# Kernel optimization log

Measured on AMD Instinct MI355X. Metric: run time of the kernel, lower is better.

## Reference

```python
import jax, jax.numpy as jnp
import numpy as np

# Static configuration matching the selected code path:
#   mode='inject_subject', is_self_attn=True, layer_id='up_blocks.0' (inject layer, bank hit)
#   alpha = AlphaScheduler.alpha(step=20, total=50, 'up_blocks.0') = 0.8 * 0.6 = 0.48
B, L, D, H = 4, 1024, 1280, 20
DH = D // H  # 64
ALPHA = 0.48


def setup_inputs() -> dict:
    key = jax.random.key(0)
    ks = jax.random.split(key, 8)
    w = lambda k, shp: (jax.random.normal(k, shp, dtype=jnp.float32) * 0.02)
    return {
        "hidden_states": jax.random.normal(ks[0], (B, L, D), dtype=jnp.float32),
        "Wq": w(ks[1], (D, D)),
        "Wk": w(ks[2], (D, D)),
        "Wv": w(ks[3], (D, D)),
        "Wo": w(ks[4], (D, D)),
        "bo": jnp.zeros((D,), dtype=jnp.float32),
        # cached background K/V, stored after head_to_batch_dim -> [B*H, L_bg, DH]
        "K_bg": jax.random.normal(ks[5], (B * H, L, DH), dtype=jnp.float32),
        "V_bg": jax.random.normal(ks[6], (B * H, L, DH), dtype=jnp.float32),
    }


def _head_to_batch(x):  # [B, L, D] -> [B*H, L, DH]
    b, l, _ = x.shape
    return x.reshape(b, l, H, DH).transpose(0, 2, 1, 3).reshape(b * H, l, DH)


def _batch_to_head(x):  # [B*H, L, DH] -> [B, L, D]
    bh, l, _ = x.shape
    b = bh // H
    return x.reshape(b, H, l, DH).transpose(0, 2, 1, 3).reshape(b, l, D)


def reference(hidden_states, Wq, Wk, Wv, Wo, bo, K_bg, V_bg):
    # q/k/v projections (self-attention: k, v from hidden_states)
    q = _head_to_batch(hidden_states @ Wq)  # [B*H, L, DH]
    k = _head_to_batch(hidden_states @ Wk)
    v = _head_to_batch(hidden_states @ Wv)

    # inject_subject: concat cached background K/V scaled by alpha along kv-seq dim
    k = jnp.concatenate([k, ALPHA * K_bg], axis=1)  # [B*H, 2L, DH]
    v = jnp.concatenate([v, ALPHA * V_bg], axis=1)

    # _sdpa: q scaled by scale*sqrt(dh), SDPA divides by sqrt(dh) -> net factor `scale`
    scale = 1.0 / jnp.sqrt(jnp.asarray(DH, dtype=q.dtype))
    scores = jnp.einsum('bqd,bkd->bqk', q, k) * scale  # [B*H, L, 2L]
    probs = jax.nn.softmax(scores, axis=-1)
    context = jnp.einsum('bqk,bkd->bqd', probs, v)  # [B*H, L, DH]

    out = _batch_to_head(context) @ Wo + bo  # to_out[0] linear
    return out
```

## Files before the change

kernel.cpp:

```cpp
#include <hip/hip_runtime.h>
#include <hip/hip_bf16.h>

#define B_   4
#define L_   1024
#define D_   1280
#define H_   20
#define DH_  64
#define BH_  (B_*H_)
#define L2_  (2*L_)
#define ALPHA_ 0.48f
#define QSCALE_ 0.180336880f

typedef __attribute__((ext_vector_type(8))) short short8;
typedef __attribute__((ext_vector_type(4))) float float4v;

__device__ __forceinline__ float exp2_fast(float x) {
    float r;
    asm volatile("v_exp_f32 %0, %1" : "=v"(r) : "v"(x));
    return r;
}

__device__ __forceinline__ ushort f2bf(float f) {
    union { float f; unsigned int i; } v; v.f = f;
    unsigned int i = v.i;
    unsigned int r = i + 0x7FFF + ((i >> 16) & 1);
    return (ushort)(r >> 16);
}
__device__ __forceinline__ short8 pack8(float4 f0, float4 f1) {
    short8 o;
    o[0] = (short)f2bf(f0.x); o[1] = (short)f2bf(f0.y);
    o[2] = (short)f2bf(f0.z); o[3] = (short)f2bf(f0.w);
    o[4] = (short)f2bf(f1.x); o[5] = (short)f2bf(f1.y);
    o[6] = (short)f2bf(f1.z); o[7] = (short)f2bf(f1.w);
    return o;
}
__device__ __forceinline__ void pack4_store(ushort* dst, float a, float b, float c, float d) {
    union { __hip_bfloat162 h; unsigned int u; } x, y;
    x.h = __float22bfloat162_rn(make_float2(a, b));
    y.h = __float22bfloat162_rn(make_float2(c, d));
    uint2 v; v.x = x.u; v.y = y.u;
    *(uint2*)dst = v;
}

__device__ __forceinline__ void async16(const void* g, void* l) {
    __builtin_amdgcn_global_load_lds(
        (__attribute__((address_space(1))) void*)g,
        (__attribute__((address_space(3))) void*)l, 16, 0, 0);
}

__global__ __launch_bounds__(256) void prep(
    const float* __restrict__ w0, const float* __restrict__ w1,
    const float* __restrict__ w2, const float* __restrict__ w3,
    ushort* __restrict__ Wt,
    const float* __restrict__ Vbg, ushort* __restrict__ Vt,
    const float* __restrict__ X, ushort* __restrict__ Xb,
    const float* __restrict__ Kbg, ushort* __restrict__ Kcv) {
    int bi = blockIdx.x, tid = threadIdx.x;
    __shared__ __align__(16) ushort t[64 * 72];
    if (bi < 2880) {
        bool doScale = (bi >= 1600);
        const float* src; int srcld; long sbase;
        ushort* dst = nullptr; int dstld = 0; long dbase = 0;
        ushort* vout = nullptr;
        if (bi < 1600) {
            int z = bi / 400, t4 = bi % 400;
            int by = t4 / 20, bx = t4 % 20;
            const float* srcs[4] = {w0, w1, w2, w3};
            src = srcs[z]; srcld = D_; dstld = D_;
            sbase = (long)(by * 64) * D_ + bx * 64;
            dst = Wt + (long)z * D_ * D_;
            dbase = (long)(bx * 64) * D_ + by * 64;
        } else {
            int j = bi - 1600;
            int bh = j >> 4, kt = j & 15;
            src = Vbg; srcld = DH_;
            sbase = ((long)bh * L_ + kt * 64) * DH_;
            vout = Vt + (((long)bh * 32 + 16 + kt) << 12);
        }
        int ldr = tid >> 3, ldc = (tid & 7) * 8;
#pragma unroll
        for (int i = 0; i < 2; i++) {
            int y = ldr + 32 * i;
            long idx = sbase + (long)y * srcld + ldc;
            float4 f0 = *(const float4*)&src[idx];
            float4 f1 = *(const float4*)&src[idx + 4];
            if (doScale) {
                f0.x *= ALPHA_; f0.y *= ALPHA_; f0.z *= ALPHA_; f0.w *= ALPHA_;
                f1.x *= ALPHA_; f1.y *= ALPHA_; f1.z *= ALPHA_; f1.w *= ALPHA_;
            }
            *(short8*)&t[y * 72 + ldc] = pack8(f0, f1);
        }
        __syncthreads();
        if (bi < 1600) {
            int r8 = (tid & 7) * 8, c0 = tid >> 3;
#pragma unroll
            for (int i = 0; i < 2; i++) {
                int c = c0 + i * 32;
                short8 o;
#pragma unroll
                for (int j2 = 0; j2 < 8; j2++) o[j2] = (short)t[(r8 + j2) * 72 + c];
                *(short8*)&dst[dbase + (long)c * dstld + r8] = o;
            }
        } else {
#pragma unroll
            for (int i = 0; i < 2; i++) {
                int jj = i * 256 + tid;
                int cc = jj >> 6, d2 = jj & 63;
                int rb = (cc >> 2) * 32 + (cc & 3) * 4;
                short8 o;
#pragma unroll
                for (int e = 0; e < 8; e++)
                    o[e] = (short)t[(rb + (e >> 2) * 16 + (e & 3)) * 72 + d2];
                *(short8*)&vout[(long)jj * 8] = o;
            }
        }
    } else if (bi < 5440) {
        long i = ((long)(bi - 2880) * 256 + tid) * 8;
        *(short8*)&Xb[i] = pack8(*(const float4*)&X[i], *(const float4*)&X[i + 4]);
    } else {
        int j2 = bi - 5440;
        int bh = j2 >> 4, kt = j2 & 15;
        const float* src = Kbg + ((long)bh * L_ + kt * 64) * DH_;
#pragma unroll
        for (int i = 0; i < 2; i++) {
            int r = i * 256 + tid;
            int kv = r >> 3, cd = r & 7;
            long idx = (long)kv * 64 + cd * 8;
            *(short8*)&t[kv * 72 + cd * 8] =
                pack8(*(const float4*)&src[idx], *(const float4*)&src[idx + 4]);
        }
        __syncthreads();
        ushort* outp = Kcv + (((long)bh * 16 + kt) << 12);
#pragma unroll
        for (int i = 0; i < 2; i++) {
            int jj = i * 256 + tid;
            int c = jj >> 6, kv = jj & 63;
            *(short8*)&outp[(long)jj * 8] = *(const short8*)&t[kv * 72 + c * 8];
        }
    }
}

template<int BMt, int BNt, int WROWS, int WCOLS>
__global__ __launch_bounds__(256) void gemm_tpl(
    const ushort* __restrict__ A, const ushort* __restrict__ Bt,
    ushort* __restrict__ Qp, ushort* __restrict__ Kp, ushort* __restrict__ Vt,
    float* __restrict__ Out, const float* __restrict__ bo, int mode) {
    constexpr int MI = BMt / WROWS / 16;
    constexpr int NI = BNt / WCOLS / 16;
    constexpr int ASZ = BMt * 32, BSZ = BNt * 32;
    constexpr int RB = 1280 / BNt;
    __shared__ __align__(16) ushort Al[2 * ASZ];
    __shared__ __align__(16) ushort Bl[2 * BSZ];
    int tid = threadIdx.x;
    int bx = blockIdx.x, by = blockIdx.y;
    int w = tid >> 6, lane = tid & 63, l15 = lane & 15, quad = lane >> 4;
    int wm = (w / WCOLS) * (BMt / WROWS);
    int wn = (w % WCOLS) * (BNt / WCOLS);
    float4v acc[MI][NI] = {};
    const int K = 1280;
    constexpr int NK = 40;
    const ushort* Arow = A + (long)by * BMt * K + (tid >> 2) * K + (tid & 3) * 8;
    const ushort* Brow = Bt + (long)bx * BNt * K + (tid >> 2) * K + (tid & 3) * 8;

    auto stage = [&](int ki, int b) {
#pragma unroll
        for (int i = 0; i < BMt / 64; i++)
            async16(Arow + (long)i * 64 * K + ki * 32, &Al[b * ASZ + (i * 4 + w) * 512]);
#pragma unroll
        for (int i = 0; i < BNt / 64; i++)
            async16(Brow + (long)i * 64 * K + ki * 32, &Bl[b * BSZ + (i * 4 + w) * 512]);
    };

    stage(0, 0);
    __syncthreads();
    for (int ki = 0; ki < NK; ki++) {
        int cur = ki & 1;
        if (ki + 1 < NK) stage(ki + 1, 1 - cur);
        short8 av[MI], bv[NI];
#pragma unroll
        for (int mi = 0; mi < MI; mi++)
            av[mi] = *(const short8*)&Al[cur * ASZ + (wm + mi * 16 + l15) * 32 + quad * 8];
#pragma unroll
        for (int ni = 0; ni < NI; ni++)
            bv[ni] = *(const short8*)&Bl[cur * BSZ + (wn + ni * 16 + l15) * 32 + quad * 8];
#pragma unroll
        for (int mi = 0; mi < MI; mi++)
#pragma unroll
            for (int ni = 0; ni < NI; ni++)
                acc[mi][ni] = __builtin_amdgcn_mfma_f32_16x16x32_bf16(av[mi], bv[ni], acc[mi][ni], 0, 0, 0);
        __syncthreads();
    }

    if (mode == 0) {
        int which = bx / RB;
#pragma unroll
        for (int mi = 0; mi < MI; mi++) {
            int m0 = by * BMt + wm + mi * 16 + quad * 4;
            int b = m0 >> 10, l0 = m0 & 1023;
#pragma unroll
            for (int ni = 0; ni < NI; ni++) {
                int n = bx * BNt + wn + ni * 16 + l15;
                int np = n - which * 1280;
                int h = np >> 6, dh = np & 63;
                if (which == 0) {
#pragma unroll
                    for (int r = 0; r < 4; r++)
                        Qp[((long)(b * H_ + h) * L_ + l0 + r) * DH_ + dh] =
                            f2bf(acc[mi][ni][r] * QSCALE_);
                } else if (which == 1) {
                    long kb = ((((long)(b * H_ + h) * 16 + (l0 >> 6)) * 8 + (dh >> 3)) * 64
                               + (l0 & 63)) * 8 + (dh & 7);
#pragma unroll
                    for (int r = 0; r < 4; r++)
                        Kp[kb + r * 8] = f2bf(acc[mi][ni][r]);
                } else {
                    int j = l0 & 63;
                    int cc = ((j >> 5) << 2) | ((j >> 2) & 3);
                    int eb = ((j >> 4) & 1) << 2;
                    pack4_store(&Vt[((((long)(b * H_ + h) * 32 + (l0 >> 6)) * 8
                                      + cc) * 64 + dh) * 8 + eb],
                                acc[mi][ni][0], acc[mi][ni][1],
                                acc[mi][ni][2], acc[mi][ni][3]);
                }
            }
        }
    } else {
#pragma unroll
        for (int mi = 0; mi < MI; mi++) {
            int mloc = wm + mi * 16 + quad * 4;
#pragma unroll
            for (int ni = 0; ni < NI; ni++) {
                int nloc = wn + ni * 16 + l15;
#pragma unroll
                for (int r = 0; r < 4; r++) {
                    int m = by * BMt + mloc + r;
                    int n = bx * BNt + nloc;
                    Out[(long)m * D_ + n] = acc[mi][ni][r] + bo[n];
                }
            }
        }
    }
}

__global__ __launch_bounds__(256) void flash_attn(
    const ushort* __restrict__ Qp, const ushort* __restrict__ Kp,
    const ushort* __restrict__ Kbg, const ushort* __restrict__ Vt,
    ushort* __restrict__ Ctx) {
    __shared__ __align__(16) ushort Kl[2 * 4096], Vl[2 * 4096];
    int tid = threadIdx.x;
    int w = tid >> 6, lane = tid & 63, l15 = lane & 15, quad = lane >> 4;
    int bi = blockIdx.x;
    int bh = (bi & 7) * 10 + ((bi >> 3) % 10);
    int qt = bi / 80;

    short8 aq[2][2];
    const ushort* Qb = Qp + ((long)bh * L_ + qt * 128 + w * 32) * DH_;
#pragma unroll
    for (int mi = 0; mi < 2; mi++)
#pragma unroll
        for (int ks = 0; ks < 2; ks++)
            aq[mi][ks] = *(const short8*)&Qb[(mi * 16 + l15) * DH_ + ks * 32 + quad * 8];

    float rs[2] = {0.f, 0.f};
    float4v O[2][4] = {};

    auto stage = [&](int kt, int b) {
        const ushort* Ksrc = (kt < 16)
            ? Kp  + (((long)bh * 16 + kt) << 12)
            : Kbg + (((long)bh * 16 + (kt - 16)) << 12);
        const ushort* Vsrc = Vt + (((long)bh * 32 + kt) << 12);
#pragma unroll
        for (int i = 0; i < 2; i++) {
            int c = w * 2 + i;
            async16(&Ksrc[c * 512 + lane * 8], &Kl[b * 4096 + c * 512]);
            async16(&Vsrc[c * 512 + lane * 8], &Vl[b * 4096 + c * 512]);
        }
    };

    stage(0, 0);
    __syncthreads();
    for (int kt = 0; kt < 32; kt++) {
        int cur = kt & 1;
        if (kt + 1 < 32) stage(kt + 1, 1 - cur);
        bool bg = (kt >= 16);
        float4v s4[4][2] = {};
#pragma unroll
        for (int ks = 0; ks < 2; ks++) {
            short8 bk[4];
#pragma unroll
            for (int nt = 0; nt < 4; nt++)
                bk[nt] = *(const short8*)&Kl[cur * 4096 + (ks * 4 + quad) * 512 + (nt * 16 + l15) * 8];
#pragma unroll
            for (int nt = 0; nt < 4; nt++)
#pragma unroll
                for (int mi = 0; mi < 2; mi++)
                    s4[nt][mi] = __builtin_amdgcn_mfma_f32_16x16x32_bf16(bk[nt], aq[mi][ks], s4[nt][mi], 0, 0, 0);
        }
        short8 ap[2][2];
#pragma unroll
        for (int mi = 0; mi < 2; mi++) {
            float p[4][4];
#pragma unroll
            for (int nt = 0; nt < 4; nt++)
#pragma unroll
                for (int r = 0; r < 4; r++) {
                    float sv = s4[nt][mi][r];
                    if (bg) sv *= ALPHA_;
                    p[nt][r] = exp2_fast(sv);
                    rs[mi] += p[nt][r];
                }
#pragma unroll
            for (int ks = 0; ks < 2; ks++) {
                float4 f0 = make_float4(p[2 * ks][0], p[2 * ks][1],
                                        p[2 * ks][2], p[2 * ks][3]);
                float4 f1 = make_float4(p[2 * ks + 1][0], p[2 * ks + 1][1],
                                        p[2 * ks + 1][2], p[2 * ks + 1][3]);
                ap[mi][ks] = pack8(f0, f1);
            }
        }
#pragma unroll
        for (int ks = 0; ks < 2; ks++) {
            short8 bv[4];
#pragma unroll
            for (int nt = 0; nt < 4; nt++)
                bv[nt] = *(const short8*)&Vl[cur * 4096 + (ks * 4 + quad) * 512 + (nt * 16 + l15) * 8];
#pragma unroll
            for (int nt = 0; nt < 4; nt++)
#pragma unroll
                for (int mi = 0; mi < 2; mi++)
                    O[mi][nt] = __builtin_amdgcn_mfma_f32_16x16x32_bf16(bv[nt], ap[mi][ks], O[mi][nt], 0, 0, 0);
        }
        __syncthreads();
    }
    int b = bh / H_, h = bh % H_;
#pragma unroll
    for (int mi = 0; mi < 2; mi++) {
        float v = rs[mi];
        v += __shfl_xor(v, 16);
        v += __shfl_xor(v, 32);
        float rcp = 1.f / v;
        long l = qt * 128 + w * 32 + mi * 16 + l15;
#pragma unroll
        for (int nt = 0; nt < 4; nt++)
            pack4_store(&Ctx[(long)(b * L_ + l) * D_ + h * DH_ + nt * 16 + quad * 4],
                        O[mi][nt][0] * rcp, O[mi][nt][1] * rcp,
                        O[mi][nt][2] * rcp, O[mi][nt][3] * rcp);
    }
}

extern "C" void kernel_launch(void* const* d_in, const int* in_sizes, int n_in,
                              void* d_out, int out_size, void* d_ws, size_t ws_size,
                              hipStream_t stream) {
    const float* X   = (const float*)d_in[0];
    const float* Wq  = (const float*)d_in[1];
    const float* Wk  = (const float*)d_in[2];
    const float* Wv  = (const float*)d_in[3];
    const float* Wo  = (const float*)d_in[4];
    const float* bo  = (const float*)d_in[5];
    const float* Kbg = (const float*)d_in[6];
    const float* Vbg = (const float*)d_in[7];

    char* ws = (char*)d_ws;
    size_t off = 0;
    auto alloc = [&](size_t bytes) {
        void* p = ws + off;
        off = (off + bytes + 255) & ~(size_t)255;
        return p;
    };
    ushort* Wt    = (ushort*)alloc((size_t)4 * D_ * D_ * 2);
    ushort* Qp    = (ushort*)alloc((size_t)BH_ * L_ * DH_ * 2);
    ushort* Kp    = (ushort*)alloc((size_t)BH_ * L_ * DH_ * 2);
    ushort* Kcv   = (ushort*)alloc((size_t)BH_ * L_ * DH_ * 2);
    ushort* Vt    = (ushort*)alloc((size_t)BH_ * DH_ * L2_ * 2);
    ushort* Xb    = (ushort*)alloc((size_t)B_ * L_ * D_ * 2);
    ushort* Ctx   = Xb;
    ushort* Wqkv_t = Wt;
    ushort* Wo_t   = Wt + (size_t)3 * D_ * D_;

    prep<<<6720, 256, 0, stream>>>(Wq, Wk, Wv, Wo, Wt, Vbg, Vt, X, Xb, Kbg, Kcv);
    gemm_tpl<128, 128, 2, 2><<<dim3(30, 32), 256, 0, stream>>>(
        Xb, Wqkv_t, Qp, Kp, Vt, nullptr, nullptr, 0);
    flash_attn<<<dim3(640), 256, 0, stream>>>(Qp, Kp, Kcv, Vt, Ctx);
    gemm_tpl<64, 128, 1, 4><<<dim3(10, 64), 256, 0, stream>>>(
        Ctx, Wo_t, nullptr, nullptr, nullptr, (float*)d_out, bo, 1);
}
```

Before: 310.0 us.

## Halve attention query tile per block and double grid size

Each wave in the flash-attention kernel now handles 16 query rows instead of 32, so a block covers 64 queries and the grid grows from 640 to 1280 blocks. This spreads the attention over more blocks and cuts per-thread register use (accumulators and Q fragments), which should raise occupancy. The cost is that each K/V tile staged into shared memory is reused by half as many queries, doubling global K/V traffic. The probability packing also switches from the custom pack8 to the __float22bfloat162_rn intrinsic.

```diff
diff --git a/kernel.cpp b/kernel.cpp
--- a/kernel.cpp
+++ b/kernel.cpp
@@ -253,16 +253,14 @@
     int bh = (bi & 7) * 10 + ((bi >> 3) % 10);
     int qt = bi / 80;
 
-    short8 aq[2][2];
-    const ushort* Qb = Qp + ((long)bh * L_ + qt * 128 + w * 32) * DH_;
-#pragma unroll
-    for (int mi = 0; mi < 2; mi++)
-#pragma unroll
-        for (int ks = 0; ks < 2; ks++)
-            aq[mi][ks] = *(const short8*)&Qb[(mi * 16 + l15) * DH_ + ks * 32 + quad * 8];
-
-    float rs[2] = {0.f, 0.f};
-    float4v O[2][4] = {};
+    short8 aq[2];
+    const ushort* Qb = Qp + ((long)bh * L_ + qt * 64 + w * 16) * DH_;
+#pragma unroll
+    for (int ks = 0; ks < 2; ks++)
+        aq[ks] = *(const short8*)&Qb[l15 * DH_ + ks * 32 + quad * 8];
+
+    float rs = 0.f;
+    float4v O[4] = {};
 
     auto stage = [&](int kt, int b) {
         const ushort* Ksrc = (kt < 16)
@@ -283,7 +281,7 @@
         int cur = kt & 1;
         if (kt + 1 < 32) stage(kt + 1, 1 - cur);
         bool bg = (kt >= 16);
-        float4v s4[4][2] = {};
+        float4v s4[4] = {};
 #pragma unroll
         for (int ks = 0; ks < 2; ks++) {
             short8 bk[4];
@@ -292,31 +290,27 @@
                 bk[nt] = *(const short8*)&Kl[cur * 4096 + (ks * 4 + quad) * 512 + (nt * 16 + l15) * 8];
 #pragma unroll
             for (int nt = 0; nt < 4; nt++)
-#pragma unroll
-                for (int mi = 0; mi < 2; mi++)
-                    s4[nt][mi] = __builtin_amdgcn_mfma_f32_16x16x32_bf16(bk[nt], aq[mi][ks], s4[nt][mi], 0, 0, 0);
-        }
-        short8 ap[2][2];
-#pragma unroll
-        for (int mi = 0; mi < 2; mi++) {
-            float p[4][4];
-#pragma unroll
-            for (int nt = 0; nt < 4; nt++)
-#pragma unroll
-                for (int r = 0; r < 4; r++) {
-                    float sv = s4[nt][mi][r];
-                    if (bg) sv *= ALPHA_;
-                    p[nt][r] = exp2_fast(sv);
-                    rs[mi] += p[nt][r];
-                }
-#pragma unroll
-            for (int ks = 0; ks < 2; ks++) {
-                float4 f0 = make_float4(p[2 * ks][0], p[2 * ks][1],
-                                        p[2 * ks][2], p[2 * ks][3]);
-                float4 f1 = make_float4(p[2 * ks + 1][0], p[2 * ks + 1][1],
-                                        p[2 * ks + 1][2], p[2 * ks + 1][3]);
-                ap[mi][ks] = pack8(f0, f1);
-            }
+                s4[nt] = __builtin_amdgcn_mfma_f32_16x16x32_bf16(bk[nt], aq[ks], s4[nt], 0, 0, 0);
+        }
+        float p[4][4];
+#pragma unroll
+        for (int nt = 0; nt < 4; nt++)
+#pragma unroll
+            for (int r = 0; r < 4; r++) {
+                float sv = s4[nt][r];
+                if (bg) sv *= ALPHA_;
+                p[nt][r] = exp2_fast(sv);
+                rs += p[nt][r];
+            }
+        short8 ap[2];
+#pragma unroll
+        for (int ks = 0; ks < 2; ks++) {
+            union { __hip_bfloat162 h[4]; short8 s; } u;
+            u.h[0] = __float22bfloat162_rn(make_float2(p[2 * ks][0], p[2 * ks][1]));
+            u.h[1] = __float22bfloat162_rn(make_float2(p[2 * ks][2], p[2 * ks][3]));
+            u.h[2] = __float22bfloat162_rn(make_float2(p[2 * ks + 1][0], p[2 * ks + 1][1]));
+            u.h[3] = __float22bfloat162_rn(make_float2(p[2 * ks + 1][2], p[2 * ks + 1][3]));
+            ap[ks] = u.s;
         }
 #pragma unroll
         for (int ks = 0; ks < 2; ks++) {
@@ -326,26 +320,21 @@
                 bv[nt] = *(const short8*)&Vl[cur * 4096 + (ks * 4 + quad) * 512 + (nt * 16 + l15) * 8];
 #pragma unroll
             for (int nt = 0; nt < 4; nt++)
-#pragma unroll
-                for (int mi = 0; mi < 2; mi++)
-                    O[mi][nt] = __builtin_amdgcn_mfma_f32_16x16x32_bf16(bv[nt], ap[mi][ks], O[mi][nt], 0, 0, 0);
+                O[nt] = __builtin_amdgcn_mfma_f32_16x16x32_bf16(bv[nt], ap[ks], O[nt], 0, 0, 0);
         }
         __syncthreads();
     }
+    float v = rs;
+    v += __shfl_xor(v, 16);
+    v += __shfl_xor(v, 32);
+    float rcp = 1.f / v;
     int b = bh / H_, h = bh % H_;
-#pragma unroll
-    for (int mi = 0; mi < 2; mi++) {
-        float v = rs[mi];
-        v += __shfl_xor(v, 16);
-        v += __shfl_xor(v, 32);
-        float rcp = 1.f / v;
-        long l = qt * 128 + w * 32 + mi * 16 + l15;
-#pragma unroll
-        for (int nt = 0; nt < 4; nt++)
-            pack4_store(&Ctx[(long)(b * L_ + l) * D_ + h * DH_ + nt * 16 + quad * 4],
-                        O[mi][nt][0] * rcp, O[mi][nt][1] * rcp,
-                        O[mi][nt][2] * rcp, O[mi][nt][3] * rcp);
-    }
+    long l = qt * 64 + w * 16 + l15;
+#pragma unroll
+    for (int nt = 0; nt < 4; nt++)
+        pack4_store(&Ctx[(long)(b * L_ + l) * D_ + h * DH_ + nt * 16 + quad * 4],
+                    O[nt][0] * rcp, O[nt][1] * rcp,
+                    O[nt][2] * rcp, O[nt][3] * rcp);
 }
 
 extern "C" void kernel_launch(void* const* d_in, const int* in_sizes, int n_in,
@@ -380,7 +369,7 @@
     prep<<<6720, 256, 0, stream>>>(Wq, Wk, Wv, Wo, Wt, Vbg, Vt, X, Xb, Kbg, Kcv);
     gemm_tpl<128, 128, 2, 2><<<dim3(30, 32), 256, 0, stream>>>(
         Xb, Wqkv_t, Qp, Kp, Vt, nullptr, nullptr, 0);
-    flash_attn<<<dim3(640), 256, 0, stream>>>(Qp, Kp, Kcv, Vt, Ctx);
+    flash_attn<<<dim3(1280), 256, 0, stream>>>(Qp, Kp, Kcv, Vt, Ctx);
     gemm_tpl<64, 128, 1, 4><<<dim3(10, 64), 256, 0, stream>>>(
         Ctx, Wo_t, nullptr, nullptr, nullptr, (float*)d_out, bo, 1);
 }
```

After: 302.8 us. -2.3%, faster.
